# Performance work log

Measured on AMD Instinct MI355X. Metric: run time of the kernel, lower is better.

Reference implementation:

```python
import jax, jax.numpy as jnp
import numpy as np

D_MODEL = 1024
H = 16
D_K = D_MODEL // H
D_FF = 4096
EPS = 1e-6


def setup_inputs() -> dict:
    key = jax.random.key(0)
    ks = jax.random.split(key, 12)
    s = 0.02
    inp = {
        "x": jax.random.normal(ks[0], (2, 2048, D_MODEL), jnp.float32),
        # attention projection weights stored [in, out] (y = x @ W + b)
        "Wq": jax.random.normal(ks[1], (D_MODEL, D_MODEL), jnp.float32) * s,
        "bq": jnp.zeros((D_MODEL,), jnp.float32),
        "Wk": jax.random.normal(ks[2], (D_MODEL, D_MODEL), jnp.float32) * s,
        "bk": jnp.zeros((D_MODEL,), jnp.float32),
        "Wv": jax.random.normal(ks[3], (D_MODEL, D_MODEL), jnp.float32) * s,
        "bv": jnp.zeros((D_MODEL,), jnp.float32),
        "Wo": jax.random.normal(ks[4], (D_MODEL, D_MODEL), jnp.float32) * s,
        "bo": jnp.zeros((D_MODEL,), jnp.float32),
        # FFN
        "W1": jax.random.normal(ks[5], (D_MODEL, D_FF), jnp.float32) * s,
        "b1": jnp.zeros((D_FF,), jnp.float32),
        "W2": jax.random.normal(ks[6], (D_FF, D_MODEL), jnp.float32) * s,
        "b2": jnp.zeros((D_MODEL,), jnp.float32),
        # scalar LayerNorm params (as in the source: nn.Parameter(torch.ones(1)))
        "ln1_alpha": jnp.ones((1,), jnp.float32),
        "ln1_beta": jnp.ones((1,), jnp.float32),
        "ln2_alpha": jnp.ones((1,), jnp.float32),
        "ln2_beta": jnp.ones((1,), jnp.float32),
    }
    return inp


def _layernorm(x, alpha, beta):
    # Faithful to source: unbiased std (ddof=1), divide by (std + eps)
    mean = jnp.mean(x, axis=-1, keepdims=True)
    var = jnp.var(x, axis=-1, keepdims=True, ddof=1)
    std = jnp.sqrt(var)
    return alpha * (x - mean) / (std + EPS) + beta


def _mha(x, Wq, bq, Wk, bk, Wv, bv, Wo, bo):
    B, S, _ = x.shape
    q = (x @ Wq + bq).reshape(B, S, H, D_K).transpose(0, 2, 1, 3)
    k = (x @ Wk + bk).reshape(B, S, H, D_K).transpose(0, 2, 1, 3)
    v = (x @ Wv + bv).reshape(B, S, H, D_K).transpose(0, 2, 1, 3)
    # NOTE: source has no 1/sqrt(d_k) scaling
    scores = jnp.einsum('bhqd,bhkd->bhqk', q, k)
    attn = jax.nn.softmax(scores, axis=-1)
    out = jnp.einsum('bhqk,bhkd->bhqd', attn, v)
    out = out.transpose(0, 2, 1, 3).reshape(B, S, D_MODEL)
    return out @ Wo + bo


def reference(x, Wq, bq, Wk, bk, Wv, bv, Wo, bo, W1, b1, W2, b2,
              ln1_alpha, ln1_beta, ln2_alpha, ln2_beta):
    # pre-norm residual 1: self-attention (dropout=0, eval mode)
    h = x + _mha(_layernorm(x, ln1_alpha, ln1_beta), Wq, bq, Wk, bk, Wv, bv, Wo, bo)
    # pre-norm residual 2: FFN
    n = _layernorm(h, ln2_alpha, ln2_beta)
    ffn = jax.nn.relu(n @ W1 + b1) @ W2 + b2
    return h + ffn
```

## Files before the change

### kernel.cpp

```cpp
#include <hip/hip_runtime.h>

#define DMODEL 1024
#define DFF    4096
#define SEQ    2048
#define NTOK   4096
#define QKVN   3072
#define LOG2E  1.4426950408889634f

typedef unsigned short u16;
typedef short s8v __attribute__((ext_vector_type(8)));
typedef float f4v __attribute__((ext_vector_type(4)));

__device__ __forceinline__ u16 f2bf(float f) {
  union { float f; unsigned u; } c; c.f = f;
  unsigned r = c.u + 0x7fffu + ((c.u >> 16) & 1u);
  return (u16)(r >> 16);
}
__device__ __forceinline__ u16 f2bf_fast(float f) {
  union { float f; unsigned u; } c; c.f = f;
  return (u16)((c.u + 0x8000u) >> 16);
}
__device__ __forceinline__ float u2f(unsigned u) {
  union { unsigned u; float f; } c; c.u = u; return c.f;
}

typedef const __attribute__((address_space(1))) unsigned GAS;
typedef __attribute__((address_space(3))) unsigned LAS;
__device__ __forceinline__ void gl2lds16(const void* g, void* l) {
  __builtin_amdgcn_global_load_lds((GAS*)g, (LAS*)l, 16, 0, 0);
}

__device__ __forceinline__ void tr32(const float* __restrict__ W, u16* __restrict__ Wt,
                                     int K, int N, int bx, int by, float (*sh)[33],
                                     float scale) {
  int n0 = bx * 32, k0 = by * 32;
  int tx = threadIdx.x & 31, ty = threadIdx.x >> 5;
#pragma unroll
  for (int r = ty; r < 32; r += 8) sh[r][tx] = W[(size_t)(k0 + r) * N + n0 + tx];
  __syncthreads();
#pragma unroll
  for (int r = ty; r < 32; r += 8) Wt[(size_t)(n0 + r) * K + k0 + tx] = f2bf(sh[tx][r] * scale);
}

__global__ __launch_bounds__(256)
void prep(const float* __restrict__ Wq, const float* __restrict__ Wk,
          const float* __restrict__ Wv, const float* __restrict__ Wo,
          const float* __restrict__ W1, const float* __restrict__ W2,
          const float* __restrict__ bq, const float* __restrict__ bk,
          const float* __restrict__ bv,
          u16* __restrict__ wqkv_t, u16* __restrict__ wo_t,
          u16* __restrict__ w1_t, u16* __restrict__ w2_t, float* __restrict__ bqkv) {
  __shared__ float sh[32][33];
  int b = blockIdx.x;
  if (b < 1024) {
    tr32(Wq, wqkv_t, 1024, 1024, b & 31, b >> 5, sh, LOG2E);
  } else if (b < 2048) {
    b -= 1024; tr32(Wk, wqkv_t + (1u << 20), 1024, 1024, b & 31, b >> 5, sh, 1.0f);
  } else if (b < 3072) {
    b -= 2048; tr32(Wv, wqkv_t + (2u << 20), 1024, 1024, b & 31, b >> 5, sh, 1.0f);
  } else if (b < 4096) {
    b -= 3072; tr32(Wo, wo_t, 1024, 1024, b & 31, b >> 5, sh, 1.0f);
  } else if (b < 8192) {
    b -= 4096; tr32(W1, w1_t, 1024, 4096, b & 127, b >> 7, sh, 1.0f);
  } else if (b < 12288) {
    b -= 8192; tr32(W2, w2_t, 4096, 1024, b & 31, b >> 5, sh, 1.0f);
  } else {
    int t = (b - 12288) * 256 + threadIdx.x;
    float v = (t < 1024) ? bq[t] * LOG2E : (t < 2048 ? bk[t - 1024] : bv[t - 2048]);
    bqkv[t] = v;
  }
}

__global__ __launch_bounds__(256)
void ln_bf16(const float* __restrict__ X, u16* __restrict__ Y,
             const float* __restrict__ a_p, const float* __restrict__ b_p) {
  int row = blockIdx.x;
  const float4* xr = (const float4*)(X + (size_t)row * DMODEL);
  float4 v = xr[threadIdx.x];
  float s  = v.x + v.y + v.z + v.w;
  float ss = v.x * v.x + v.y * v.y + v.z * v.z + v.w * v.w;
#pragma unroll
  for (int m = 32; m >= 1; m >>= 1) { s += __shfl_xor(s, m, 64); ss += __shfl_xor(ss, m, 64); }
  __shared__ float red[8];
  int wid = threadIdx.x >> 6, lane = threadIdx.x & 63;
  if (lane == 0) { red[wid] = s; red[4 + wid] = ss; }
  __syncthreads();
  s  = red[0] + red[1] + red[2] + red[3];
  ss = red[4] + red[5] + red[6] + red[7];
  float mean = s * (1.0f / 1024.0f);
  float var  = fmaxf((ss - s * mean) * (1.0f / 1023.0f), 0.0f);
  float k    = a_p[0] / (sqrtf(var) + 1e-6f);
  float beta = b_p[0];
  ushort4 o;
  o.x = f2bf((v.x - mean) * k + beta);
  o.y = f2bf((v.y - mean) * k + beta);
  o.z = f2bf((v.z - mean) * k + beta);
  o.w = f2bf((v.w - mean) * k + beta);
  ((ushort4*)(Y + (size_t)row * DMODEL))[threadIdx.x] = o;
}

template <int RELU, int RESID, int OUT_BF16, int ATOMIC>
__global__ __launch_bounds__(256, 3)
void gemm_bt(const u16* __restrict__ A, const u16* __restrict__ Bt,
             const float* __restrict__ bias, const float* __restrict__ resid,
             void* __restrict__ Cout, int M, int N, int K) {
  __shared__ __align__(16) u16 As[128 * 64];
  __shared__ __align__(16) u16 Bs[128 * 64];
  const int lane = threadIdx.x & 63, wid = threadIdx.x >> 6;
  const int llo = lane & 15, lhi = lane >> 4;
  const int m0 = blockIdx.y * 128, n0 = blockIdx.x * 128;
  const int wm = wid & 1, wn = wid >> 1;
  const int r8 = lane >> 3;
  const int c8 = ((lane & 7) ^ r8) * 8;

  f4v acc[4][4];
  const f4v fz = {0.f, 0.f, 0.f, 0.f};
#pragma unroll
  for (int i = 0; i < 4; ++i)
#pragma unroll
    for (int j = 0; j < 4; ++j) acc[i][j] = fz;

  const u16* Ag = A  + (size_t)(m0 + r8) * K + c8;
  const u16* Bg = Bt + (size_t)(n0 + r8) * K + c8;

  const int Kp = ATOMIC ? (K / gridDim.z) : K;
  const int kbeg = ATOMIC ? blockIdx.z * Kp : 0;
  const int kend = kbeg + Kp;

  for (int kt = kbeg; kt < kend; kt += 64) {
#pragma unroll
    for (int c = 0; c < 4; ++c) {
      int ch = wid * 4 + c;
      gl2lds16(Ag + (size_t)(ch * 8) * K + kt, As + ch * 512);
      gl2lds16(Bg + (size_t)(ch * 8) * K + kt, Bs + ch * 512);
    }
    __syncthreads();
#pragma unroll
    for (int ks = 0; ks < 2; ++ks) {
      const int so = ((ks * 4 + lhi) ^ (llo & 7)) * 8;
      s8v a[4], b[4];
#pragma unroll
      for (int i = 0; i < 4; ++i)
        a[i] = *(const s8v*)&As[(wm * 64 + i * 16 + llo) * 64 + so];
#pragma unroll
      for (int j = 0; j < 4; ++j)
        b[j] = *(const s8v*)&Bs[(wn * 64 + j * 16 + llo) * 64 + so];
#pragma unroll
      for (int i = 0; i < 4; ++i)
#pragma unroll
        for (int j = 0; j < 4; ++j)
          acc[i][j] = __builtin_amdgcn_mfma_f32_16x16x32_bf16(a[i], b[j], acc[i][j], 0, 0, 0);
    }
    __syncthreads();
  }
#pragma unroll
  for (int j = 0; j < 4; ++j) {
    int col = n0 + wn * 64 + j * 16 + llo;
    float bv = bias[col];
#pragma unroll
    for (int i = 0; i < 4; ++i) {
      int r0 = m0 + wm * 64 + i * 16 + lhi * 4;
#pragma unroll
      for (int r = 0; r < 4; ++r) {
        size_t idx = (size_t)(r0 + r) * N + col;
        float v = acc[i][j][r];
        if (ATOMIC) {
          if (blockIdx.z == 0) {
            v += bv;
            if (RESID) v += resid[idx];
          }
          atomicAdd(&((float*)Cout)[idx], v);
        } else {
          v += bv;
          if (RESID) v += resid[idx];
          if (RELU) v = fmaxf(v, 0.0f);
          if (OUT_BF16) ((u16*)Cout)[idx] = f2bf(v);
          else          ((float*)Cout)[idx] = v;
        }
      }
    }
  }
}

__global__ __launch_bounds__(256, 2)
void flash_attn(const u16* __restrict__ QKV, u16* __restrict__ Pacc,
                float* __restrict__ Pml) {
  __shared__ __align__(16) u16 smem[26112];
  u16* Qs = smem;
  u16* Ks = smem + 8192;
  u16* Ps = smem;
  u16* Vt = smem + 17408;

  const int tid = threadIdx.x;
  const int lane = tid & 63, wid = tid >> 6;
  const int llo = lane & 15, lhi = lane >> 4;
  const int qt = blockIdx.x, bh = blockIdx.y, z = blockIdx.z;
  const int b = bh >> 4, h = bh & 15;
  const int LDM = QKVN;
  const size_t base = (size_t)b * SEQ * LDM + h * 64;
  const u16* Qb = QKV + base + (size_t)qt * 128 * LDM;
  const u16* Kb = QKV + base + 1024;
  const u16* Vb = QKV + base + 2048;
  const int r8 = lane >> 3;
  const int c8 = ((lane & 7) ^ r8) * 8;

#pragma unroll
  for (int c = 0; c < 4; ++c) {
    int ch = wid * 4 + c;
    gl2lds16(Qb + (size_t)(ch * 8 + r8) * LDM + c8, Qs + ch * 512);
  }
  __syncthreads();
  s8v qf[2][2];
#pragma unroll
  for (int mb = 0; mb < 2; ++mb)
#pragma unroll
    for (int ks = 0; ks < 2; ++ks)
      qf[mb][ks] = *(const s8v*)&Qs[(wid * 32 + mb * 16 + llo) * 64 +
                                    (((ks * 4 + lhi) ^ (llo & 7)) * 8)];

  f4v accO[2][4];
  float l_run[2][4];
  const f4v fz = {0.f, 0.f, 0.f, 0.f};
#pragma unroll
  for (int mb = 0; mb < 2; ++mb) {
#pragma unroll
    for (int db = 0; db < 4; ++db) accO[mb][db] = fz;
#pragma unroll
    for (int r = 0; r < 4; ++r) l_run[mb][r] = 0.f;
  }

  for (int kt = z * 8; kt < z * 8 + 8; ++kt) {
#pragma unroll
    for (int c = 0; c < 4; ++c) {
      int ch = wid * 4 + c;
      gl2lds16(Kb + (size_t)(kt * 128 + ch * 8 + r8) * LDM + c8, Ks + ch * 512);
    }
#pragma unroll
    for (int it = 0; it < 2; ++it) {
      int o  = (tid >> 6) + it * 4;
      int k2 = (tid & 63) * 2;
      const u16* vp = Vb + (size_t)(kt * 128 + k2) * LDM + o * 8;
      s8v v0 = *(const s8v*)vp;
      s8v v1 = *(const s8v*)(vp + LDM);
      const u16* e0 = (const u16*)&v0;
      const u16* e1 = (const u16*)&v1;
#pragma unroll
      for (int j = 0; j < 8; ++j) {
        unsigned pk = (unsigned)e0[j] | ((unsigned)e1[j] << 16);
        *(unsigned*)&Vt[(o * 8 + j) * 136 + k2] = pk;
      }
    }
    __syncthreads();

    f4v accS[2][8];
#pragma unroll
    for (int mb = 0; mb < 2; ++mb)
#pragma unroll
      for (int nb = 0; nb < 8; ++nb) accS[mb][nb] = fz;
#pragma unroll
    for (int ks = 0; ks < 2; ++ks) {
      const int so = ((ks * 4 + lhi) ^ (llo & 7)) * 8;
      s8v kf[8];
#pragma unroll
      for (int nb = 0; nb < 8; ++nb)
        kf[nb] = *(const s8v*)&Ks[(nb * 16 + llo) * 64 + so];
#pragma unroll
      for (int mb = 0; mb < 2; ++mb)
#pragma unroll
        for (int nb = 0; nb < 8; ++nb)
          accS[mb][nb] = __builtin_amdgcn_mfma_f32_16x16x32_bf16(qf[mb][ks], kf[nb], accS[mb][nb], 0, 0, 0);
    }
    __syncthreads();

#pragma unroll
    for (int mb = 0; mb < 2; ++mb)
#pragma unroll
      for (int nb = 0; nb < 8; ++nb)
#pragma unroll
        for (int r = 0; r < 4; ++r) {
          float p = __builtin_amdgcn_exp2f(accS[mb][nb][r]);
          l_run[mb][r] += p;
          Ps[(size_t)(wid * 32 + mb * 16 + lhi * 4 + r) * 136 + nb * 16 + llo] = f2bf_fast(p);
        }
    __syncthreads();

#pragma unroll
    for (int ks = 0; ks < 4; ++ks) {
      s8v pa[2], vb2[4];
#pragma unroll
      for (int mb = 0; mb < 2; ++mb)
        pa[mb] = *(const s8v*)&Ps[(wid * 32 + mb * 16 + llo) * 136 + ks * 32 + lhi * 8];
#pragma unroll
      for (int db = 0; db < 4; ++db)
        vb2[db] = *(const s8v*)&Vt[(db * 16 + llo) * 136 + ks * 32 + lhi * 8];
#pragma unroll
      for (int mb = 0; mb < 2; ++mb)
#pragma unroll
        for (int db = 0; db < 4; ++db)
          accO[mb][db] = __builtin_amdgcn_mfma_f32_16x16x32_bf16(pa[mb], vb2[db], accO[mb][db], 0, 0, 0);
    }
    __syncthreads();
  }

#pragma unroll
  for (int mb = 0; mb < 2; ++mb)
#pragma unroll
    for (int r = 0; r < 4; ++r)
#pragma unroll
      for (int sh = 1; sh < 16; sh <<= 1)
        l_run[mb][r] += __shfl_xor(l_run[mb][r], sh, 64);

#pragma unroll
  for (int mb = 0; mb < 2; ++mb)
#pragma unroll
    for (int r = 0; r < 4; ++r) {
      int row = qt * 128 + wid * 32 + mb * 16 + lhi * 4 + r;
      size_t ibase = (size_t)(z * 32 + bh) * SEQ + row;
      if (llo == 0) Pml[ibase] = l_run[mb][r];
#pragma unroll
      for (int db = 0; db < 4; ++db)
        Pacc[ibase * 64 + db * 16 + llo] = f2bf(accO[mb][db][r]);
    }
}

__global__ __launch_bounds__(256)
void attn_combine(const u16* __restrict__ Pacc, const float* __restrict__ Pml,
                  u16* __restrict__ ctx) {
  int g = blockIdx.x * 256 + threadIdx.x;
  int d2 = g & 31;
  int row = (g >> 5) & (SEQ - 1);
  int bh = g >> 16;
  int b = bh >> 4, h = bh & 15;
  size_t i0 = (size_t)bh * SEQ + row;
  size_t i1 = (size_t)(32 + bh) * SEQ + row;
  float inv = 1.0f / (Pml[i0] + Pml[i1]);
  unsigned pa = ((const unsigned*)Pacc)[i0 * 32 + d2];
  unsigned pb = ((const unsigned*)Pacc)[i1 * 32 + d2];
  float lo = u2f(pa << 16) + u2f(pb << 16);
  float hi = u2f(pa & 0xffff0000u) + u2f(pb & 0xffff0000u);
  unsigned o = (unsigned)f2bf(lo * inv) | ((unsigned)f2bf(hi * inv) << 16);
  ((unsigned*)ctx)[(size_t)(b * SEQ + row) * (DMODEL / 2) + h * 32 + d2] = o;
}

extern "C" void kernel_launch(void* const* d_in, const int* in_sizes, int n_in,
                              void* d_out, int out_size, void* d_ws, size_t ws_size,
                              hipStream_t stream) {
  const float* x   = (const float*)d_in[0];
  const float* Wq  = (const float*)d_in[1];  const float* bq = (const float*)d_in[2];
  const float* Wk  = (const float*)d_in[3];  const float* bk = (const float*)d_in[4];
  const float* Wv  = (const float*)d_in[5];  const float* bv = (const float*)d_in[6];
  const float* Wo  = (const float*)d_in[7];  const float* bo = (const float*)d_in[8];
  const float* W1  = (const float*)d_in[9];  const float* b1 = (const float*)d_in[10];
  const float* W2  = (const float*)d_in[11]; const float* b2 = (const float*)d_in[12];
  const float* l1a = (const float*)d_in[13]; const float* l1b = (const float*)d_in[14];
  const float* l2a = (const float*)d_in[15]; const float* l2b = (const float*)d_in[16];

  char* ws = (char*)d_ws;
  const size_t MB = 1u << 20;
  u16*   wqkv_t = (u16*)(ws + 0);
  u16*   wo_t   = (u16*)(ws + 6 * MB);
  u16*   w1_t   = (u16*)(ws + 8 * MB);
  u16*   w2_t   = (u16*)(ws + 16 * MB);
  float* bqkv   = (float*)(ws + 24 * MB);
  u16*   xn1    = (u16*)(ws + 25 * MB);
  u16*   qkv    = (u16*)(ws + 33 * MB);
  u16*   ctx    = (u16*)(ws + 57 * MB);
  float* hbuf   = (float*)(ws + 65 * MB);
  u16*   Pacc   = (u16*)(ws + 81 * MB);
  float* Pml    = (float*)(ws + 97 * MB);
  u16*   n2     = (u16*)(ws + 81 * MB);
  u16*   mid    = (u16*)(ws + 25 * MB);

  dim3 blk(256);

  hipMemsetAsync(d_out, 0, (size_t)NTOK * DMODEL * 4, stream);
  hipMemsetAsync(hbuf, 0, (size_t)NTOK * DMODEL * 4, stream);

  prep<<<dim3(12300), blk, 0, stream>>>(Wq, Wk, Wv, Wo, W1, W2, bq, bk, bv,
                                        wqkv_t, wo_t, w1_t, w2_t, bqkv);

  ln_bf16<<<NTOK, blk, 0, stream>>>(x, xn1, l1a, l1b);

  gemm_bt<0, 0, 1, 0><<<dim3(24, 32), blk, 0, stream>>>(xn1, wqkv_t, bqkv, nullptr, qkv,
                                                        NTOK, QKVN, DMODEL);

  flash_attn<<<dim3(16, 32, 2), blk, 0, stream>>>(qkv, Pacc, Pml);
  attn_combine<<<dim3(8192), blk, 0, stream>>>(Pacc, Pml, ctx);

  gemm_bt<0, 1, 0, 1><<<dim3(8, 32, 2), blk, 0, stream>>>(ctx, wo_t, bo, x, hbuf,
                                                          NTOK, DMODEL, DMODEL);

  ln_bf16<<<NTOK, blk, 0, stream>>>(hbuf, n2, l2a, l2b);

  gemm_bt<1, 0, 1, 0><<<dim3(32, 32), blk, 0, stream>>>(n2, w1_t, b1, nullptr, mid,
                                                        NTOK, DFF, DMODEL);

  gemm_bt<0, 1, 0, 1><<<dim3(8, 32, 2), blk, 0, stream>>>(mid, w2_t, b2, hbuf, (float*)d_out,
                                                          NTOK, DMODEL, DFF);
}
```

Measured before the change: 410.7 us.

## Keep attention probabilities in registers via transposed QK^T and permlane swaps

Computes S^T by swapping MFMA operand order so each lane holds a key-column strip, then exponentiates, packs to bf16 with v_cvt_pk_bf16_f32, and uses permlane32/16 swaps to form the A-operand layout for the PV MFMA directly. This removes the P round-trip through LDS along with two block barriers per key tile, shrinks shared memory, and raises the occupancy hint to 3 blocks. The row-sum reduction becomes cheaper because each lane now owns one query row. The risks are register pressure under the tighter launch bound and correctness of the lane-permutation layout.

```diff
diff --git a/kernel.cpp b/kernel.cpp
--- a/kernel.cpp
+++ b/kernel.cpp
@@ -16,12 +16,20 @@
   unsigned r = c.u + 0x7fffu + ((c.u >> 16) & 1u);
   return (u16)(r >> 16);
 }
-__device__ __forceinline__ u16 f2bf_fast(float f) {
-  union { float f; unsigned u; } c; c.f = f;
-  return (u16)((c.u + 0x8000u) >> 16);
-}
 __device__ __forceinline__ float u2f(unsigned u) {
   union { unsigned u; float f; } c; c.u = u; return c.f;
+}
+
+__device__ __forceinline__ unsigned cvt_pk_bf16(float lo, float hi) {
+  unsigned r;
+  asm("v_cvt_pk_bf16_f32 %0, %1, %2" : "=v"(r) : "v"(lo), "v"(hi));
+  return r;
+}
+__device__ __forceinline__ void pl32swap(unsigned& x, unsigned& y) {
+  asm("v_permlane32_swap_b32 %0, %1" : "+v"(x), "+v"(y));
+}
+__device__ __forceinline__ void pl16swap(unsigned& x, unsigned& y) {
+  asm("v_permlane16_swap_b32 %0, %1" : "+v"(x), "+v"(y));
 }
 
 typedef const __attribute__((address_space(1))) unsigned GAS;
@@ -182,14 +190,12 @@
   }
 }
 
-__global__ __launch_bounds__(256, 2)
+__global__ __launch_bounds__(256, 3)
 void flash_attn(const u16* __restrict__ QKV, u16* __restrict__ Pacc,
                 float* __restrict__ Pml) {
-  __shared__ __align__(16) u16 smem[26112];
-  u16* Qs = smem;
-  u16* Ks = smem + 8192;
-  u16* Ps = smem;
-  u16* Vt = smem + 17408;
+  __shared__ __align__(16) u16 smem[16896];
+  u16* Ks = smem;
+  u16* Vt = smem + 8192;
 
   const int tid = threadIdx.x;
   const int lane = tid & 63, wid = tid >> 6;
@@ -207,7 +213,7 @@
 #pragma unroll
   for (int c = 0; c < 4; ++c) {
     int ch = wid * 4 + c;
-    gl2lds16(Qb + (size_t)(ch * 8 + r8) * LDM + c8, Qs + ch * 512);
+    gl2lds16(Qb + (size_t)(ch * 8 + r8) * LDM + c8, Ks + ch * 512);
   }
   __syncthreads();
   s8v qf[2][2];
@@ -215,19 +221,17 @@
   for (int mb = 0; mb < 2; ++mb)
 #pragma unroll
     for (int ks = 0; ks < 2; ++ks)
-      qf[mb][ks] = *(const s8v*)&Qs[(wid * 32 + mb * 16 + llo) * 64 +
+      qf[mb][ks] = *(const s8v*)&Ks[(wid * 32 + mb * 16 + llo) * 64 +
                                     (((ks * 4 + lhi) ^ (llo & 7)) * 8)];
+  __syncthreads();
 
   f4v accO[2][4];
-  float l_run[2][4];
+  float l_run[2] = {0.f, 0.f};
   const f4v fz = {0.f, 0.f, 0.f, 0.f};
 #pragma unroll
-  for (int mb = 0; mb < 2; ++mb) {
+  for (int mb = 0; mb < 2; ++mb)
 #pragma unroll
     for (int db = 0; db < 4; ++db) accO[mb][db] = fz;
-#pragma unroll
-    for (int r = 0; r < 4; ++r) l_run[mb][r] = 0.f;
-  }
 
   for (int kt = z * 8; kt < z * 8 + 8; ++kt) {
 #pragma unroll
@@ -237,8 +241,8 @@
     }
 #pragma unroll
     for (int it = 0; it < 2; ++it) {
-      int o  = (tid >> 6) + it * 4;
-      int k2 = (tid & 63) * 2;
+      int o  = wid + it * 4;
+      int k2 = lane * 2;
       const u16* vp = Vb + (size_t)(kt * 128 + k2) * LDM + o * 8;
       s8v v0 = *(const s8v*)vp;
       s8v v1 = *(const s8v*)(vp + LDM);
@@ -252,44 +256,47 @@
     }
     __syncthreads();
 
-    f4v accS[2][8];
-#pragma unroll
-    for (int mb = 0; mb < 2; ++mb)
-#pragma unroll
-      for (int nb = 0; nb < 8; ++nb) accS[mb][nb] = fz;
-#pragma unroll
-    for (int ks = 0; ks < 2; ++ks) {
-      const int so = ((ks * 4 + lhi) ^ (llo & 7)) * 8;
-      s8v kf[8];
-#pragma unroll
-      for (int nb = 0; nb < 8; ++nb)
-        kf[nb] = *(const s8v*)&Ks[(nb * 16 + llo) * 64 + so];
-#pragma unroll
-      for (int mb = 0; mb < 2; ++mb)
-#pragma unroll
-        for (int nb = 0; nb < 8; ++nb)
-          accS[mb][nb] = __builtin_amdgcn_mfma_f32_16x16x32_bf16(qf[mb][ks], kf[nb], accS[mb][nb], 0, 0, 0);
-    }
-    __syncthreads();
-
-#pragma unroll
-    for (int mb = 0; mb < 2; ++mb)
-#pragma unroll
-      for (int nb = 0; nb < 8; ++nb)
-#pragma unroll
-        for (int r = 0; r < 4; ++r) {
-          float p = __builtin_amdgcn_exp2f(accS[mb][nb][r]);
-          l_run[mb][r] += p;
-          Ps[(size_t)(wid * 32 + mb * 16 + lhi * 4 + r) * 136 + nb * 16 + llo] = f2bf_fast(p);
+    s8v pa[2][4];
+#pragma unroll
+    for (int ksb = 0; ksb < 4; ++ksb) {
+      f4v sA[2], sB[2];
+#pragma unroll
+      for (int mb = 0; mb < 2; ++mb) { sA[mb] = fz; sB[mb] = fz; }
+#pragma unroll
+      for (int ks = 0; ks < 2; ++ks) {
+        const int so = ((ks * 4 + lhi) ^ (llo & 7)) * 8;
+        s8v kfA = *(const s8v*)&Ks[((ksb * 2 + 0) * 16 + llo) * 64 + so];
+        s8v kfB = *(const s8v*)&Ks[((ksb * 2 + 1) * 16 + llo) * 64 + so];
+#pragma unroll
+        for (int mb = 0; mb < 2; ++mb) {
+          sA[mb] = __builtin_amdgcn_mfma_f32_16x16x32_bf16(kfA, qf[mb][ks], sA[mb], 0, 0, 0);
+          sB[mb] = __builtin_amdgcn_mfma_f32_16x16x32_bf16(kfB, qf[mb][ks], sB[mb], 0, 0, 0);
         }
-    __syncthreads();
+      }
+#pragma unroll
+      for (int mb = 0; mb < 2; ++mb) {
+        float pA0 = __builtin_amdgcn_exp2f(sA[mb][0]);
+        float pA1 = __builtin_amdgcn_exp2f(sA[mb][1]);
+        float pA2 = __builtin_amdgcn_exp2f(sA[mb][2]);
+        float pA3 = __builtin_amdgcn_exp2f(sA[mb][3]);
+        float pB0 = __builtin_amdgcn_exp2f(sB[mb][0]);
+        float pB1 = __builtin_amdgcn_exp2f(sB[mb][1]);
+        float pB2 = __builtin_amdgcn_exp2f(sB[mb][2]);
+        float pB3 = __builtin_amdgcn_exp2f(sB[mb][3]);
+        l_run[mb] += ((pA0 + pA1) + (pA2 + pA3)) + ((pB0 + pB1) + (pB2 + pB3));
+        unsigned a0 = cvt_pk_bf16(pA0, pA1), a1 = cvt_pk_bf16(pA2, pA3);
+        unsigned b0 = cvt_pk_bf16(pB0, pB1), b1 = cvt_pk_bf16(pB2, pB3);
+        pl32swap(a0, b0); pl16swap(a0, b0);
+        pl32swap(a1, b1); pl16swap(a1, b1);
+        union { unsigned u[4]; s8v v; } pk;
+        pk.u[0] = a0; pk.u[1] = a1; pk.u[2] = b0; pk.u[3] = b1;
+        pa[mb][ksb] = pk.v;
+      }
+    }
 
 #pragma unroll
     for (int ks = 0; ks < 4; ++ks) {
-      s8v pa[2], vb2[4];
-#pragma unroll
-      for (int mb = 0; mb < 2; ++mb)
-        pa[mb] = *(const s8v*)&Ps[(wid * 32 + mb * 16 + llo) * 136 + ks * 32 + lhi * 8];
+      s8v vb2[4];
 #pragma unroll
       for (int db = 0; db < 4; ++db)
         vb2[db] = *(const s8v*)&Vt[(db * 16 + llo) * 136 + ks * 32 + lhi * 8];
@@ -297,30 +304,29 @@
       for (int mb = 0; mb < 2; ++mb)
 #pragma unroll
         for (int db = 0; db < 4; ++db)
-          accO[mb][db] = __builtin_amdgcn_mfma_f32_16x16x32_bf16(pa[mb], vb2[db], accO[mb][db], 0, 0, 0);
+          accO[mb][db] = __builtin_amdgcn_mfma_f32_16x16x32_bf16(pa[mb][ks], vb2[db], accO[mb][db], 0, 0, 0);
     }
     __syncthreads();
   }
 
 #pragma unroll
-  for (int mb = 0; mb < 2; ++mb)
-#pragma unroll
-    for (int r = 0; r < 4; ++r)
-#pragma unroll
-      for (int sh = 1; sh < 16; sh <<= 1)
-        l_run[mb][r] += __shfl_xor(l_run[mb][r], sh, 64);
-
-#pragma unroll
-  for (int mb = 0; mb < 2; ++mb)
+  for (int mb = 0; mb < 2; ++mb) {
+    l_run[mb] += __shfl_xor(l_run[mb], 16, 64);
+    l_run[mb] += __shfl_xor(l_run[mb], 32, 64);
+  }
+#pragma unroll
+  for (int mb = 0; mb < 2; ++mb) {
+    int row0 = qt * 128 + wid * 32 + mb * 16;
+    size_t ibase = (size_t)(z * 32 + bh) * SEQ + row0;
+    if (lane < 16) Pml[ibase + lane] = l_run[mb];
 #pragma unroll
     for (int r = 0; r < 4; ++r) {
-      int row = qt * 128 + wid * 32 + mb * 16 + lhi * 4 + r;
-      size_t ibase = (size_t)(z * 32 + bh) * SEQ + row;
-      if (llo == 0) Pml[ibase] = l_run[mb][r];
+      size_t irow = ibase + lhi * 4 + r;
 #pragma unroll
       for (int db = 0; db < 4; ++db)
-        Pacc[ibase * 64 + db * 16 + llo] = f2bf(accO[mb][db][r]);
-    }
+        Pacc[irow * 64 + db * 16 + llo] = f2bf(accO[mb][db][r]);
+    }
+  }
 }
 
 __global__ __launch_bounds__(256)
```

Measured after the change: 396.2 us. 1.04x faster.
